# Performance work log

Measured on AMD Instinct MI355X. Metric: run time of the kernel, lower is better.

Reference implementation:

```python
import jax, jax.numpy as jnp
import numpy as np

N = 50000      # nodes
E = 800000     # edges
F_IN = 128     # num_features
H = 64         # hidden_dim
G = 64         # graphs in batch
EPS = 1e-5


def setup_inputs() -> dict:
    ks = jax.random.split(jax.random.key(0), 16)
    x = jax.random.normal(ks[0], (N, F_IN), dtype=jnp.float32)
    edge_index = jax.random.randint(ks[1], (2, E), 0, N, dtype=jnp.int64)
    batch = jnp.sort(jax.random.randint(ks[2], (N,), 0, G, dtype=jnp.int64))
    s = 0.05
    inp = {"x": x, "edge_index": edge_index, "batch": batch}
    # GCNConv layers: W [out,in], bias [out]; BatchNorm gamma/beta [H]
    dims = [(H, F_IN), (H, H), (H, H)]
    for i, (o, ci) in enumerate(dims):
        inp[f"W{i}"] = jax.random.normal(ks[3 + i], (o, ci), dtype=jnp.float32) * s
        inp[f"b{i}"] = jnp.zeros((o,), dtype=jnp.float32)
        inp[f"g{i}"] = jnp.ones((o,), dtype=jnp.float32)
        inp[f"be{i}"] = jnp.zeros((o,), dtype=jnp.float32)
    inp["lin1_w"] = jax.random.normal(ks[10], (H // 2, H), dtype=jnp.float32) * s
    inp["lin1_b"] = jnp.zeros((H // 2,), dtype=jnp.float32)
    inp["lin2_w"] = jax.random.normal(ks[11], (1, H // 2), dtype=jnp.float32) * s
    inp["lin2_b"] = jnp.zeros((1,), dtype=jnp.float32)
    return inp


def _gcn_conv(x, src, dst, W, b):
    # PyG GCNConv: h = x W^T; add self-loops; symmetric deg^{-1/2} norm; scatter-add; + bias
    h = x @ W.T                                   # [N, out]
    n = x.shape[0]
    deg = jax.ops.segment_sum(jnp.ones(src.shape[0], h.dtype), dst, num_segments=n) + 1.0
    dinv = jax.lax.rsqrt(deg)                     # [N]
    msg = h[src] * (dinv[src] * dinv[dst])[:, None]   # per-edge messages
    agg = jax.ops.segment_sum(msg, dst, num_segments=n)
    agg = agg + h * (dinv * dinv)[:, None]        # self-loop contribution
    return agg + b


def _bn_relu(x, g, be):
    # BatchNorm1d (training-mode batch stats, biased var) + ReLU; dropout = identity (eval)
    m = x.mean(axis=0)
    v = jnp.var(x, axis=0)
    return jax.nn.relu((x - m) * jax.lax.rsqrt(v + EPS) * g + be)


def reference(x, edge_index, batch,
              W0, b0, g0, be0, W1, b1, g1, be1, W2, b2, g2, be2,
              lin1_w, lin1_b, lin2_w, lin2_b):
    src, dst = edge_index[0], edge_index[1]
    Ws = [(W0, b0, g0, be0), (W1, b1, g1, be1), (W2, b2, g2, be2)]
    h = x
    for (W, b, g, be) in Ws:
        h = _bn_relu(_gcn_conv(h, src, dst, W, b), g, be)
    # global mean pool over graphs
    sums = jax.ops.segment_sum(h, batch, num_segments=G)          # [G, H]
    cnt = jax.ops.segment_sum(jnp.ones((h.shape[0],), h.dtype), batch, num_segments=G)
    pooled = sums / jnp.maximum(cnt, 1.0)[:, None]
    h = jax.nn.relu(pooled @ lin1_w.T + lin1_b)
    return h @ lin2_w.T + lin2_b                                   # [G, 1]
```

## Files before the change

### kernel.cpp

```cpp
#include <hip/hip_runtime.h>

#define NN 50000
#define NE 800000
#define FIN 128
#define H 64
#define NG 64
#define BN_EPS 1e-5f
#define INV_N (1.0f / 50000.0f)
#define NBKT 196
#define PB 256
#define SLICE 64
#define BKCAP 8192
#define PROWS 16
#define NSEG 4

__device__ __forceinline__ void f4acc(float4& a, const float4 b) {
    a.x += b.x; a.y += b.y; a.z += b.z; a.w += b.w;
}
__device__ __forceinline__ void f4accw(float4& a, const float4 b, float w) {
    a.x += b.x * w; a.y += b.y * w; a.z += b.z * w; a.w += b.w * w;
}

__global__ void prep(const float* __restrict__ W0, const float* __restrict__ W1,
                     const float* __restrict__ W2, const int* __restrict__ src,
                     const int* __restrict__ dst, float* __restrict__ Wt0,
                     float* __restrict__ Wt1, float* __restrict__ Wt2,
                     float* __restrict__ sl0, float* __restrict__ sl1,
                     float* __restrict__ sl2, float* __restrict__ pool,
                     float* __restrict__ cnt, int* __restrict__ cnts,
                     unsigned int* __restrict__ staged) {
    const int tid = threadIdx.x, bid = blockIdx.x;
    const int gtid = bid * 256 + tid;
    const int gsz = PB * 256;
    for (int i = gtid; i < 64 * 128; i += gsz) { sl0[i] = 0.f; sl1[i] = 0.f; sl2[i] = 0.f; }
    for (int i = gtid; i < NG * H; i += gsz) pool[i] = 0.f;
    if (gtid < NG) cnt[gtid] = 0.f;
    for (int i = gtid; i < FIN * 64; i += gsz) {
        int k = i >> 6, o = i & 63;
        Wt0[i] = W0[o * FIN + k];
    }
    for (int i = gtid; i < H * 64; i += gsz) {
        int k = i >> 6, o = i & 63;
        Wt1[i] = W1[o * H + k];
        Wt2[i] = W2[o * H + k];
    }
    __shared__ int hcnt[NBKT];
    for (int i = tid; i < NBKT; i += 256) hcnt[i] = 0;
    __syncthreads();
    const int chunk = NE / PB;
    const int e0 = bid * chunk, e1 = e0 + chunk;
    for (int e = e0 + tid; e < e1; e += 256) {
        int d = dst[e];
        int s = src[e];
        int bkt = d >> 8;
        int idx = atomicAdd(&hcnt[bkt], 1);
        if (idx < SLICE)
            staged[(size_t)(bkt * PB + bid) * SLICE + idx] =
                (unsigned int)s | ((unsigned int)(d & 255) << 16);
    }
    __syncthreads();
    for (int i = tid; i < NBKT; i += 256) cnts[i * PB + bid] = min(hcnt[i], SLICE);
}

union CsrMmSh {
    struct { float Xs[64 * 68]; float Ws[64 * 64]; } mm;
    struct { int cnt[256]; int loc[256]; int cur[256]; int spre[257]; } csr;
};

__device__ __forceinline__ int slice_find(const int* __restrict__ spre, int t) {
    int lo = 0, hi = 255;
    while (lo < hi) {
        int mid = (lo + hi + 1) >> 1;
        if (spre[mid] <= t) lo = mid; else hi = mid - 1;
    }
    return lo;
}

template <int K, bool SEGIN>
__device__ __forceinline__ void mm_tile_body(int base, const float* __restrict__ x,
                                             const float* __restrict__ Wtg,
                                             const float* __restrict__ slots,
                                             const float* __restrict__ gamma,
                                             const float* __restrict__ beta,
                                             const float* __restrict__ dv,
                                             float* __restrict__ outp, float* Xs, float* Ws,
                                             float* st, int n) {
    const int tid = threadIdx.x;
    if (slots) {
        if (tid < 128) {
            float s0 = 0.f, s1 = 0.f, s2 = 0.f, s3 = 0.f;
            for (int k = 0; k < 64; k += 4) {
                s0 += slots[(k + 0) * 128 + tid];
                s1 += slots[(k + 1) * 128 + tid];
                s2 += slots[(k + 2) * 128 + tid];
                s3 += slots[(k + 3) * 128 + tid];
            }
            st[tid] = (s0 + s1) + (s2 + s3);
        }
        __syncthreads();
    }
    const int q = tid >> 4;
    const int co = (tid & 15) * 4;
    const int kq = (tid & 15) * 4;
    float4 a0 = make_float4(0.f, 0.f, 0.f, 0.f);
    float4 a1 = a0, a2 = a0, a3 = a0;

    for (int kc = 0; kc < K; kc += 64) {
        if (kc) __syncthreads();
        for (int i = tid; i < 64 * 64; i += 256) Ws[i] = Wtg[kc * 64 + i];
        {
            const int kidx = kc + kq;
            float4 sc = make_float4(1.f, 1.f, 1.f, 1.f);
            float4 sh = make_float4(0.f, 0.f, 0.f, 0.f);
            if (slots) {
                float4 s = *(const float4*)&st[kidx];
                float4 ss = *(const float4*)&st[64 + kidx];
                float4 gm = *(const float4*)&gamma[kidx];
                float4 bt = *(const float4*)&beta[kidx];
                float mx = s.x * INV_N, my = s.y * INV_N, mz = s.z * INV_N, mw = s.w * INV_N;
                sc.x = gm.x * rsqrtf(ss.x * INV_N - mx * mx + BN_EPS);
                sc.y = gm.y * rsqrtf(ss.y * INV_N - my * my + BN_EPS);
                sc.z = gm.z * rsqrtf(ss.z * INV_N - mz * mz + BN_EPS);
                sc.w = gm.w * rsqrtf(ss.w * INV_N - mw * mw + BN_EPS);
                sh.x = bt.x - mx * sc.x;
                sh.y = bt.y - my * sc.y;
                sh.z = bt.z - mz * sc.z;
                sh.w = bt.w - mw * sc.w;
            }
            for (int j = 0; j < 4; ++j) {
                int r = (tid >> 4) + j * 16;
                int row = base + r;
                float4 v = make_float4(0.f, 0.f, 0.f, 0.f);
                if (row < n) {
                    if (SEGIN)
                        v = *(const float4*)&x[((size_t)(kidx >> 4) * NN + row) * 16 + (kidx & 15)];
                    else
                        v = *(const float4*)&x[(size_t)row * K + kidx];
                }
                if (slots) {
                    v.x = fmaxf(v.x * sc.x + sh.x, 0.f);
                    v.y = fmaxf(v.y * sc.y + sh.y, 0.f);
                    v.z = fmaxf(v.z * sc.z + sh.z, 0.f);
                    v.w = fmaxf(v.w * sc.w + sh.w, 0.f);
                }
                *(float4*)&Xs[r * 68 + kq] = v;
            }
        }
        __syncthreads();

#pragma unroll 2
        for (int k = 0; k < 64; k += 4) {
            float4 x0 = *(const float4*)&Xs[(q + 0) * 68 + k];
            float4 x1 = *(const float4*)&Xs[(q + 16) * 68 + k];
            float4 x2 = *(const float4*)&Xs[(q + 32) * 68 + k];
            float4 x3 = *(const float4*)&Xs[(q + 48) * 68 + k];
            float4 w0 = *(const float4*)&Ws[(k + 0) * 64 + co];
            float4 w1 = *(const float4*)&Ws[(k + 1) * 64 + co];
            float4 w2 = *(const float4*)&Ws[(k + 2) * 64 + co];
            float4 w3 = *(const float4*)&Ws[(k + 3) * 64 + co];

            a0.x += x0.x * w0.x + x0.y * w1.x + x0.z * w2.x + x0.w * w3.x;
            a0.y += x0.x * w0.y + x0.y * w1.y + x0.z * w2.y + x0.w * w3.y;
            a0.z += x0.x * w0.z + x0.y * w1.z + x0.z * w2.z + x0.w * w3.z;
            a0.w += x0.x * w0.w + x0.y * w1.w + x0.z * w2.w + x0.w * w3.w;

            a1.x += x1.x * w0.x + x1.y * w1.x + x1.z * w2.x + x1.w * w3.x;
            a1.y += x1.x * w0.y + x1.y * w1.y + x1.z * w2.y + x1.w * w3.y;
            a1.z += x1.x * w0.z + x1.y * w1.z + x1.z * w2.z + x1.w * w3.z;
            a1.w += x1.x * w0.w + x1.y * w1.w + x1.z * w2.w + x1.w * w3.w;

            a2.x += x2.x * w0.x + x2.y * w1.x + x2.z * w2.x + x2.w * w3.x;
            a2.y += x2.x * w0.y + x2.y * w1.y + x2.z * w2.y + x2.w * w3.y;
            a2.z += x2.x * w0.z + x2.y * w1.z + x2.z * w2.z + x2.w * w3.z;
            a2.w += x2.x * w0.w + x2.y * w1.w + x2.z * w2.w + x2.w * w3.w;

            a3.x += x3.x * w0.x + x3.y * w1.x + x3.z * w2.x + x3.w * w3.x;
            a3.y += x3.x * w0.y + x3.y * w1.y + x3.z * w2.y + x3.w * w3.y;
            a3.z += x3.x * w0.z + x3.y * w1.z + x3.z * w2.z + x3.w * w3.z;
            a3.w += x3.x * w0.w + x3.y * w1.w + x3.z * w2.w + x3.w * w3.w;
        }
    }

    const int sg = co >> 4, so = co & 15;
    int r0 = base + q;
    if (r0 < n) {
        float d = dv ? dv[r0] : 1.f;
        a0.x *= d; a0.y *= d; a0.z *= d; a0.w *= d;
        *(float4*)&outp[((size_t)sg * NN + r0) * 16 + so] = a0;
    }
    if (r0 + 16 < n) {
        float d = dv ? dv[r0 + 16] : 1.f;
        a1.x *= d; a1.y *= d; a1.z *= d; a1.w *= d;
        *(float4*)&outp[((size_t)sg * NN + r0 + 16) * 16 + so] = a1;
    }
    if (r0 + 32 < n) {
        float d = dv ? dv[r0 + 32] : 1.f;
        a2.x *= d; a2.y *= d; a2.z *= d; a2.w *= d;
        *(float4*)&outp[((size_t)sg * NN + r0 + 32) * 16 + so] = a2;
    }
    if (r0 + 48 < n) {
        float d = dv ? dv[r0 + 48] : 1.f;
        a3.x *= d; a3.y *= d; a3.z *= d; a3.w *= d;
        *(float4*)&outp[((size_t)sg * NN + r0 + 48) * 16 + so] = a3;
    }
}

__global__ __launch_bounds__(256, 4) void csr_mm0(
    const unsigned int* __restrict__ staged, const int* __restrict__ cnts,
    int* __restrict__ rs, int* __restrict__ re, float* __restrict__ dinv,
    int* __restrict__ csr, const float* __restrict__ x, const float* __restrict__ Wt0,
    float* __restrict__ bufA) {
    __shared__ CsrMmSh sh;
    const int tid = threadIdx.x;
    if (blockIdx.x < NBKT) {
        const int b = blockIdx.x;
        int c = cnts[b * PB + tid];
        sh.csr.loc[tid] = c;
        sh.csr.cnt[tid] = 0;
        __syncthreads();
        for (int off = 1; off < 256; off <<= 1) {
            int t = (tid >= off) ? sh.csr.loc[tid - off] : 0;
            __syncthreads();
            sh.csr.loc[tid] += t;
            __syncthreads();
        }
        sh.csr.spre[tid] = sh.csr.loc[tid] - c;
        if (tid == 255) sh.csr.spre[256] = sh.csr.loc[255];
        __syncthreads();
        const int T = sh.csr.spre[256];
        for (int t = tid; t < T; t += 256) {
            int s = slice_find(sh.csr.spre, t);
            unsigned int u = staged[(size_t)(b * PB + s) * SLICE + (t - sh.csr.spre[s])];
            atomicAdd(&sh.csr.cnt[(u >> 16) & 255], 1);
        }
        __syncthreads();
        int v = sh.csr.cnt[tid];
        sh.csr.loc[tid] = v;
        __syncthreads();
        for (int off = 1; off < 256; off <<= 1) {
            int t = (tid >= off) ? sh.csr.loc[tid - off] : 0;
            __syncthreads();
            sh.csr.loc[tid] += t;
            __syncthreads();
        }
        const int start = b * BKCAP + sh.csr.loc[tid] - v;
        const int node = b * 256 + tid;
        if (node < NN) {
            rs[node] = start;
            re[node] = start + v;
            dinv[node] = rsqrtf((float)v + 1.0f);
        }
        sh.csr.cur[tid] = start;
        __syncthreads();
        for (int t = tid; t < T; t += 256) {
            int s = slice_find(sh.csr.spre, t);
            unsigned int u = staged[(size_t)(b * PB + s) * SLICE + (t - sh.csr.spre[s])];
            int j = atomicAdd(&sh.csr.cur[(u >> 16) & 255], 1);
            csr[j] = (int)(u & 0xFFFFu);
        }
    } else {
        mm_tile_body<FIN, false>((blockIdx.x - NBKT) * 64, x, Wt0, nullptr, nullptr, nullptr,
                                 nullptr, bufA, sh.mm.Xs, sh.mm.Ws, nullptr, NN);
    }
}

__global__ __launch_bounds__(256, 4) void matmul_bn(const float* __restrict__ x,
                                                    const float* __restrict__ Wtg,
                                                    const float* __restrict__ slots,
                                                    const float* __restrict__ gamma,
                                                    const float* __restrict__ beta,
                                                    const float* __restrict__ dv,
                                                    float* __restrict__ outp, int n) {
    __shared__ float Xs[64 * 68];
    __shared__ float Ws[64 * 64];
    __shared__ __align__(16) float st[128];
    mm_tile_body<H, true>(blockIdx.x * 64, x, Wtg, slots, gamma, beta, dv, outp, Xs, Ws, st, n);
}

template <bool ED>
__global__ __launch_bounds__(256) void gather_seg(const float* __restrict__ h,
                                                  const int* __restrict__ rs,
                                                  const int* __restrict__ re,
                                                  const int* __restrict__ csrc,
                                                  const float* __restrict__ dv,
                                                  const float* __restrict__ bias,
                                                  float* __restrict__ outp,
                                                  float* __restrict__ slots, int seg) {
    const int tid = threadIdx.x;
    const int wv = tid >> 6;
    const int lane = tid & 63;
    const int fl = lane & 3;
    const int ss = (lane >> 2) & 3;
    const int ds = lane >> 4;
    const int d = (blockIdx.x * 4 + wv) * 4 + ds;
    const float* hseg = h + (size_t)seg * NN * 16;
    const int fo = fl * 4;
    const int j1 = re[d];
    const float dA = dv[d];
    float4 acc = make_float4(0.f, 0.f, 0.f, 0.f);
    int j = rs[d] + ss;
    while (j + 4 < j1) {
        int s0 = csrc[j], s1 = csrc[j + 4];
        if (ED) {
            f4accw(acc, *(const float4*)&hseg[(size_t)s0 * 16 + fo], dv[s0]);
            f4accw(acc, *(const float4*)&hseg[(size_t)s1 * 16 + fo], dv[s1]);
        } else {
            f4acc(acc, *(const float4*)&hseg[(size_t)s0 * 16 + fo]);
            f4acc(acc, *(const float4*)&hseg[(size_t)s1 * 16 + fo]);
        }
        j += 8;
    }
    if (j < j1) {
        int s0 = csrc[j];
        if (ED)
            f4accw(acc, *(const float4*)&hseg[(size_t)s0 * 16 + fo], dv[s0]);
        else
            f4acc(acc, *(const float4*)&hseg[(size_t)s0 * 16 + fo]);
    }
    acc.x += __shfl_xor(acc.x, 4); acc.x += __shfl_xor(acc.x, 8);
    acc.y += __shfl_xor(acc.y, 4); acc.y += __shfl_xor(acc.y, 8);
    acc.z += __shfl_xor(acc.z, 4); acc.z += __shfl_xor(acc.z, 8);
    acc.w += __shfl_xor(acc.w, 4); acc.w += __shfl_xor(acc.w, 8);
    const float4 self = *(const float4*)&hseg[(size_t)d * 16 + fo];
    const float4 bq = *(const float4*)&bias[seg * 16 + fo];
    const float sf = ED ? dA : 1.f;
    float4 v;
    v.x = bq.x + dA * (acc.x + sf * self.x);
    v.y = bq.y + dA * (acc.y + sf * self.y);
    v.z = bq.z + dA * (acc.z + sf * self.z);
    v.w = bq.w + dA * (acc.w + sf * self.w);
    if (ss == 0) *(float4*)&outp[((size_t)seg * NN + d) * 16 + fo] = v;
    __shared__ float4 red[2][4][4][4];
    if (ss == 0) {
        float4 vq;
        vq.x = v.x * v.x; vq.y = v.y * v.y; vq.z = v.z * v.z; vq.w = v.w * v.w;
        red[0][wv][ds][fl] = v;
        red[1][wv][ds][fl] = vq;
    }
    __syncthreads();
    if (tid < 8) {
        int a = tid >> 2, f2 = tid & 3;
        float4 s = make_float4(0.f, 0.f, 0.f, 0.f);
#pragma unroll
        for (int i = 0; i < 16; ++i) f4acc(s, red[a][i >> 2][i & 3][f2]);
        float* slot = slots + (blockIdx.x & 63) * 128 + a * 64 + seg * 16 + f2 * 4;
        atomicAdd(&slot[0], s.x);
        atomicAdd(&slot[1], s.y);
        atomicAdd(&slot[2], s.z);
        atomicAdd(&slot[3], s.w);
    }
}

__global__ void pool_seg(const float* __restrict__ h, const float* __restrict__ slots,
                         const float* __restrict__ gamma, const float* __restrict__ beta,
                         const int* __restrict__ batch, float* __restrict__ pool,
                         float* __restrict__ cnt, int n) {
    __shared__ __align__(16) float pst[128];
    if (threadIdx.x < 128) {
        float s0 = 0.f, s1 = 0.f, s2 = 0.f, s3 = 0.f;
        for (int k = 0; k < 64; k += 4) {
            s0 += slots[(k + 0) * 128 + threadIdx.x];
            s1 += slots[(k + 1) * 128 + threadIdx.x];
            s2 += slots[(k + 2) * 128 + threadIdx.x];
            s3 += slots[(k + 3) * 128 + threadIdx.x];
        }
        pst[threadIdx.x] = (s0 + s1) + (s2 + s3);
    }
    __syncthreads();
    int wave = blockIdx.x * 4 + (threadIdx.x >> 6);
    int c = threadIdx.x & 63;
    int r0 = wave * PROWS;
    if (r0 >= n) return;
    int r1 = min(r0 + PROWS, n);
    float mean = pst[c] * INV_N;
    float var = pst[64 + c] * INV_N - mean * mean;
    float sc = gamma[c] * rsqrtf(var + BN_EPS);
    float sh = beta[c] - mean * sc;
    const size_t segbase = (size_t)(c >> 4) * NN * 16 + (c & 15);
    int cur = batch[r0];
    float acc = 0.f;
    int nlocal = 0;
    for (int r = r0; r < r1; ++r) {
        int g = batch[r];
        if (g != cur) {
            atomicAdd(&pool[cur * H + c], acc);
            if (c == 0) atomicAdd(&cnt[cur], (float)nlocal);
            cur = g;
            acc = 0.f;
            nlocal = 0;
        }
        acc += fmaxf(h[segbase + (size_t)r * 16] * sc + sh, 0.f);
        ++nlocal;
    }
    atomicAdd(&pool[cur * H + c], acc);
    if (c == 0) atomicAdd(&cnt[cur], (float)nlocal);
}

__global__ void final_mlp(const float* __restrict__ pool, const float* __restrict__ cnt,
                          const float* __restrict__ l1w, const float* __restrict__ l1b,
                          const float* __restrict__ l2w, const float* __restrict__ l2b,
                          float* __restrict__ out) {
    int tid = blockIdx.x * 256 + threadIdx.x;
    int g = tid >> 5;
    int j = tid & 31;
    if (g >= NG) return;
    float inv = 1.0f / fmaxf(cnt[g], 1.0f);
    float s = l1b[j];
    for (int k = 0; k < H; ++k) s += pool[g * H + k] * inv * l1w[j * H + k];
    float v = fmaxf(s, 0.0f) * l2w[j];
    for (int off = 16; off > 0; off >>= 1) v += __shfl_down(v, off, 32);
    if (j == 0) out[g] = v + l2b[0];
}

extern "C" void kernel_launch(void* const* d_in, const int* in_sizes, int n_in,
                              void* d_out, int out_size, void* d_ws, size_t ws_size,
                              hipStream_t stream) {
    const float* x = (const float*)d_in[0];
    const int* ei = (const int*)d_in[1];
    const int* batch = (const int*)d_in[2];
    const float* W[3] = {(const float*)d_in[3], (const float*)d_in[7], (const float*)d_in[11]};
    const float* b[3] = {(const float*)d_in[4], (const float*)d_in[8], (const float*)d_in[12]};
    const float* g[3] = {(const float*)d_in[5], (const float*)d_in[9], (const float*)d_in[13]};
    const float* be[3] = {(const float*)d_in[6], (const float*)d_in[10], (const float*)d_in[14]};
    const float* l1w = (const float*)d_in[15];
    const float* l1b = (const float*)d_in[16];
    const float* l2w = (const float*)d_in[17];
    const float* l2b = (const float*)d_in[18];
    float* out = (float*)d_out;

    const int* src = ei;
    const int* dst = ei + NE;

    char* wsb = (char*)d_ws;
    size_t off = 0;
    auto alloc = [&](size_t elems) {
        void* p = wsb + off;
        off += elems * 4;
        return p;
    };
    float* dinv = (float*)alloc(50048);
    float* bufA = (float*)alloc((size_t)NN * H);
    float* bufB = (float*)alloc((size_t)NN * H);
    float* slots[3] = {(float*)alloc(64 * 128), (float*)alloc(64 * 128), (float*)alloc(64 * 128)};
    float* pool = (float*)alloc(NG * H);
    float* cnt = (float*)alloc(64);
    float* Wt[3] = {(float*)alloc(FIN * 64), (float*)alloc(H * 64), (float*)alloc(H * 64)};
    int* rs = (int*)alloc(50048);
    int* re = (int*)alloc(50048);
    int* cnts = (int*)alloc((size_t)NBKT * PB);
    unsigned int* staged = (unsigned int*)alloc((size_t)NBKT * PB * SLICE);
    int* csr = (int*)alloc((size_t)NBKT * BKCAP);

    const int grid_mm = (NN + 63) / 64;
    const int grid_gs = NN / 16;

    prep<<<PB, 256, 0, stream>>>(W[0], W[1], W[2], src, dst, Wt[0], Wt[1], Wt[2], slots[0],
                                 slots[1], slots[2], pool, cnt, cnts, staged);
    csr_mm0<<<NBKT + grid_mm, 256, 0, stream>>>(staged, cnts, rs, re, dinv, csr, x, Wt[0], bufA);
    for (int s = 0; s < NSEG; ++s)
        gather_seg<true><<<grid_gs, 256, 0, stream>>>(bufA, rs, re, csr, dinv, b[0], bufB,
                                                      slots[0], s);
    matmul_bn<<<grid_mm, 256, 0, stream>>>(bufB, Wt[1], slots[0], g[0], be[0], dinv, bufA, NN);
    for (int s = 0; s < NSEG; ++s)
        gather_seg<false><<<grid_gs, 256, 0, stream>>>(bufA, rs, re, csr, dinv, b[1], bufB,
                                                       slots[1], s);
    matmul_bn<<<grid_mm, 256, 0, stream>>>(bufB, Wt[2], slots[1], g[1], be[1], dinv, bufA, NN);
    for (int s = 0; s < NSEG; ++s)
        gather_seg<false><<<grid_gs, 256, 0, stream>>>(bufA, rs, re, csr, dinv, b[2], bufB,
                                                       slots[2], s);
    const int pool_grid = ((NN + PROWS - 1) / PROWS + 3) / 4;
    pool_seg<<<pool_grid, 256, 0, stream>>>(bufB, slots[2], g[2], be[2], batch, pool, cnt, NN);
    final_mlp<<<8, 256, 0, stream>>>(pool, cnt, l1w, l1b, l2w, l2b, out);
}
```

Baseline: 366.6 us.

## Merge gather segment launches, shrink CSR indices to u16, add nontemporal access

Replaces the four per-segment gather launches per layer with one launch that interleaves segments across blocks. It stores CSR source indices as 16-bit values, which halves index traffic; this relies on the local index fitting in 16 bits. It also uses nontemporal loads and stores, a second accumulator for more memory-level parallelism, and a wave-shuffle reduction for the BN statistics that cuts shared-memory work. The aim is to remove launch overhead and per-edge bandwidth in the gather, at the risk of cache-behaviour changes from the nontemporal hints.

```diff
diff --git a/kernel.cpp b/kernel.cpp
--- a/kernel.cpp
+++ b/kernel.cpp
@@ -14,11 +14,16 @@
 #define PROWS 16
 #define NSEG 4
 
+typedef float f4v __attribute__((ext_vector_type(4)));
+
 __device__ __forceinline__ void f4acc(float4& a, const float4 b) {
     a.x += b.x; a.y += b.y; a.z += b.z; a.w += b.w;
 }
 __device__ __forceinline__ void f4accw(float4& a, const float4 b, float w) {
     a.x += b.x * w; a.y += b.y * w; a.z += b.z * w; a.w += b.w * w;
+}
+__device__ __forceinline__ void nt_store4(float* p, const float4 v) {
+    __builtin_nontemporal_store(*(const f4v*)&v, (f4v*)p);
 }
 
 __global__ void prep(const float* __restrict__ W0, const float* __restrict__ W1,
@@ -208,8 +213,8 @@
 __global__ __launch_bounds__(256, 4) void csr_mm0(
     const unsigned int* __restrict__ staged, const int* __restrict__ cnts,
     int* __restrict__ rs, int* __restrict__ re, float* __restrict__ dinv,
-    int* __restrict__ csr, const float* __restrict__ x, const float* __restrict__ Wt0,
-    float* __restrict__ bufA) {
+    unsigned short* __restrict__ csr, const float* __restrict__ x,
+    const float* __restrict__ Wt0, float* __restrict__ bufA) {
     __shared__ CsrMmSh sh;
     const int tid = threadIdx.x;
     if (blockIdx.x < NBKT) {
@@ -256,7 +261,7 @@
             int s = slice_find(sh.csr.spre, t);
             unsigned int u = staged[(size_t)(b * PB + s) * SLICE + (t - sh.csr.spre[s])];
             int j = atomicAdd(&sh.csr.cur[(u >> 16) & 255], 1);
-            csr[j] = (int)(u & 0xFFFFu);
+            csr[j] = (unsigned short)(u & 0xFFFFu);
         }
     } else {
         mm_tile_body<FIN, false>((blockIdx.x - NBKT) * 64, x, Wt0, nullptr, nullptr, nullptr,
@@ -278,45 +283,51 @@
 }
 
 template <bool ED>
-__global__ __launch_bounds__(256) void gather_seg(const float* __restrict__ h,
-                                                  const int* __restrict__ rs,
-                                                  const int* __restrict__ re,
-                                                  const int* __restrict__ csrc,
-                                                  const float* __restrict__ dv,
-                                                  const float* __restrict__ bias,
-                                                  float* __restrict__ outp,
-                                                  float* __restrict__ slots, int seg) {
+__global__ __launch_bounds__(256) void gather_seg4(const float* __restrict__ h,
+                                                   const int* __restrict__ rs,
+                                                   const int* __restrict__ re,
+                                                   const unsigned short* __restrict__ csrc,
+                                                   const float* __restrict__ dv,
+                                                   const float* __restrict__ bias,
+                                                   float* __restrict__ outp,
+                                                   float* __restrict__ slots) {
     const int tid = threadIdx.x;
+    const int bid = blockIdx.x;
+    const int seg = bid & 3;
     const int wv = tid >> 6;
     const int lane = tid & 63;
     const int fl = lane & 3;
     const int ss = (lane >> 2) & 3;
     const int ds = lane >> 4;
-    const int d = (blockIdx.x * 4 + wv) * 4 + ds;
+    const int d = (bid >> 2) * 16 + wv * 4 + ds;
     const float* hseg = h + (size_t)seg * NN * 16;
     const int fo = fl * 4;
-    const int j1 = re[d];
+    const int j0 = __builtin_nontemporal_load(&rs[d]);
+    const int j1 = __builtin_nontemporal_load(&re[d]);
     const float dA = dv[d];
     float4 acc = make_float4(0.f, 0.f, 0.f, 0.f);
-    int j = rs[d] + ss;
+    float4 acc2 = acc;
+    int j = j0 + ss;
     while (j + 4 < j1) {
-        int s0 = csrc[j], s1 = csrc[j + 4];
+        int s0 = __builtin_nontemporal_load(&csrc[j]);
+        int s1 = __builtin_nontemporal_load(&csrc[j + 4]);
         if (ED) {
             f4accw(acc, *(const float4*)&hseg[(size_t)s0 * 16 + fo], dv[s0]);
-            f4accw(acc, *(const float4*)&hseg[(size_t)s1 * 16 + fo], dv[s1]);
+            f4accw(acc2, *(const float4*)&hseg[(size_t)s1 * 16 + fo], dv[s1]);
         } else {
             f4acc(acc, *(const float4*)&hseg[(size_t)s0 * 16 + fo]);
-            f4acc(acc, *(const float4*)&hseg[(size_t)s1 * 16 + fo]);
+            f4acc(acc2, *(const float4*)&hseg[(size_t)s1 * 16 + fo]);
         }
         j += 8;
     }
     if (j < j1) {
-        int s0 = csrc[j];
+        int s0 = __builtin_nontemporal_load(&csrc[j]);
         if (ED)
             f4accw(acc, *(const float4*)&hseg[(size_t)s0 * 16 + fo], dv[s0]);
         else
             f4acc(acc, *(const float4*)&hseg[(size_t)s0 * 16 + fo]);
     }
+    f4acc(acc, acc2);
     acc.x += __shfl_xor(acc.x, 4); acc.x += __shfl_xor(acc.x, 8);
     acc.y += __shfl_xor(acc.y, 4); acc.y += __shfl_xor(acc.y, 8);
     acc.z += __shfl_xor(acc.z, 4); acc.z += __shfl_xor(acc.z, 8);
@@ -329,21 +340,30 @@
     v.y = bq.y + dA * (acc.y + sf * self.y);
     v.z = bq.z + dA * (acc.z + sf * self.z);
     v.w = bq.w + dA * (acc.w + sf * self.w);
-    if (ss == 0) *(float4*)&outp[((size_t)seg * NN + d) * 16 + fo] = v;
-    __shared__ float4 red[2][4][4][4];
-    if (ss == 0) {
-        float4 vq;
-        vq.x = v.x * v.x; vq.y = v.y * v.y; vq.z = v.z * v.z; vq.w = v.w * v.w;
-        red[0][wv][ds][fl] = v;
-        red[1][wv][ds][fl] = vq;
+    if (ss == 0) nt_store4(&outp[((size_t)seg * NN + d) * 16 + fo], v);
+    float4 q;
+    q.x = v.x * v.x; q.y = v.y * v.y; q.z = v.z * v.z; q.w = v.w * v.w;
+    v.x += __shfl_xor(v.x, 16); v.x += __shfl_xor(v.x, 32);
+    v.y += __shfl_xor(v.y, 16); v.y += __shfl_xor(v.y, 32);
+    v.z += __shfl_xor(v.z, 16); v.z += __shfl_xor(v.z, 32);
+    v.w += __shfl_xor(v.w, 16); v.w += __shfl_xor(v.w, 32);
+    q.x += __shfl_xor(q.x, 16); q.x += __shfl_xor(q.x, 32);
+    q.y += __shfl_xor(q.y, 16); q.y += __shfl_xor(q.y, 32);
+    q.z += __shfl_xor(q.z, 16); q.z += __shfl_xor(q.z, 32);
+    q.w += __shfl_xor(q.w, 16); q.w += __shfl_xor(q.w, 32);
+    __shared__ float4 red[2][4][4];
+    if (ss == 0 && ds == 0) {
+        red[0][wv][fl] = v;
+        red[1][wv][fl] = q;
     }
     __syncthreads();
     if (tid < 8) {
-        int a = tid >> 2, f2 = tid & 3;
-        float4 s = make_float4(0.f, 0.f, 0.f, 0.f);
-#pragma unroll
-        for (int i = 0; i < 16; ++i) f4acc(s, red[a][i >> 2][i & 3][f2]);
-        float* slot = slots + (blockIdx.x & 63) * 128 + a * 64 + seg * 16 + f2 * 4;
+        int a = tid >> 2, f = tid & 3;
+        float4 s = red[a][0][f];
+        f4acc(s, red[a][1][f]);
+        f4acc(s, red[a][2][f]);
+        f4acc(s, red[a][3][f]);
+        float* slot = slots + ((bid >> 2) & 63) * 128 + a * 64 + seg * 16 + f * 4;
         atomicAdd(&slot[0], s.x);
         atomicAdd(&slot[1], s.y);
         atomicAdd(&slot[2], s.z);
@@ -449,25 +469,19 @@
     int* re = (int*)alloc(50048);
     int* cnts = (int*)alloc((size_t)NBKT * PB);
     unsigned int* staged = (unsigned int*)alloc((size_t)NBKT * PB * SLICE);
-    int* csr = (int*)alloc((size_t)NBKT * BKCAP);
+    unsigned short* csr = (unsigned short*)alloc((size_t)NBKT * BKCAP / 2);
 
     const int grid_mm = (NN + 63) / 64;
-    const int grid_gs = NN / 16;
+    const int grid_g4 = (NN / 16) * NSEG;
 
     prep<<<PB, 256, 0, stream>>>(W[0], W[1], W[2], src, dst, Wt[0], Wt[1], Wt[2], slots[0],
                                  slots[1], slots[2], pool, cnt, cnts, staged);
     csr_mm0<<<NBKT + grid_mm, 256, 0, stream>>>(staged, cnts, rs, re, dinv, csr, x, Wt[0], bufA);
-    for (int s = 0; s < NSEG; ++s)
-        gather_seg<true><<<grid_gs, 256, 0, stream>>>(bufA, rs, re, csr, dinv, b[0], bufB,
-                                                      slots[0], s);
+    gather_seg4<true><<<grid_g4, 256, 0, stream>>>(bufA, rs, re, csr, dinv, b[0], bufB, slots[0]);
     matmul_bn<<<grid_mm, 256, 0, stream>>>(bufB, Wt[1], slots[0], g[0], be[0], dinv, bufA, NN);
-    for (int s = 0; s < NSEG; ++s)
-        gather_seg<false><<<grid_gs, 256, 0, stream>>>(bufA, rs, re, csr, dinv, b[1], bufB,
-                                                       slots[1], s);
+    gather_seg4<false><<<grid_g4, 256, 0, stream>>>(bufA, rs, re, csr, dinv, b[1], bufB, slots[1]);
     matmul_bn<<<grid_mm, 256, 0, stream>>>(bufB, Wt[2], slots[1], g[1], be[1], dinv, bufA, NN);
-    for (int s = 0; s < NSEG; ++s)
-        gather_seg<false><<<grid_gs, 256, 0, stream>>>(bufA, rs, re, csr, dinv, b[2], bufB,
-                                                       slots[2], s);
+    gather_seg4<false><<<grid_g4, 256, 0, stream>>>(bufA, rs, re, csr, dinv, b[2], bufB, slots[2]);
     const int pool_grid = ((NN + PROWS - 1) / PROWS + 3) / 4;
     pool_seg<<<pool_grid, 256, 0, stream>>>(bufB, slots[2], g[2], be[2], batch, pool, cnt, NN);
     final_mlp<<<8, 256, 0, stream>>>(pool, cnt, l1w, l1b, l2w, l2b, out);
```

After: 357.1 us. -2.6%, faster.
